# Optimization experiments

Measured on AMD Instinct MI355X. Metric: run time of the kernel, lower is better.

## Reference

```python
import jax, jax.numpy as jnp
import numpy as np

P = 1.0  # Yager t-norm exponent (tnorm_p)


def _patches(x, k):
    # x: [B, C, H, W] -> [B, C*k*k, Ho, Wo], feature ordering (c, kh, kw) like torch unfold
    B, C, H, W = x.shape
    Ho, Wo = H - k + 1, W - k + 1
    cols = [x[:, :, i:i + Ho, j:j + Wo] for i in range(k) for j in range(k)]
    p = jnp.stack(cols, axis=2)  # [B, C, k*k, Ho, Wo]
    return p.reshape(B, C * k * k, Ho, Wo)


def _max_yager2d(x, w, p):
    # Fuzzy conv: Yager t-norm T(a,b)=max(0, 1-((1-a)^p+(1-b)^p)^(1/p)) between each
    # patch element and kernel weight, aggregated with max over the receptive field.
    O, C, k, _ = w.shape
    pat = _patches(x, k)                       # [B, L, Ho, Wo], L = C*k*k
    wf = w.reshape(O, -1)                      # [O, L]
    a = 1.0 - pat[:, None]                     # [B, 1, L, Ho, Wo]
    b = 1.0 - wf[None, :, :, None, None]       # [1, O, L, 1, 1]
    t = jnp.maximum(0.0, 1.0 - (a ** p + b ** p) ** (1.0 / p))
    return jnp.max(t, axis=2)                  # [B, O, Ho, Wo]


def _maxpool2(x):
    return jax.lax.reduce_window(x, -jnp.inf, jax.lax.max,
                                 (1, 1, 2, 2), (1, 1, 2, 2), 'VALID')


def setup_inputs() -> dict:
    key = jax.random.key(0)
    k1, k2, k3, k4, k5, k6, k7 = jax.random.split(key, 7)
    B = 128
    inputs = jax.random.uniform(k1, (B, 3, 32, 32), dtype=jnp.float32)
    # fuzzy kernels are membership values in [0,1]
    w1 = jax.random.uniform(k2, (6, 3, 5, 5), dtype=jnp.float32)
    w2 = jax.random.uniform(k3, (16, 6, 5, 5), dtype=jnp.float32)
    w3 = jax.random.uniform(k4, (120, 16, 5, 5), dtype=jnp.float32)
    wd = jax.random.normal(k5, (120, 84), dtype=jnp.float32) * 0.1  # DenseDefuzzy weights
    wf = jax.random.normal(k6, (84, 10), dtype=jnp.float32) * 0.1   # fc5 weight
    bf = jax.random.normal(k7, (10,), dtype=jnp.float32) * 0.01     # fc5 bias
    return {"inputs": inputs, "w1": w1, "w2": w2, "w3": w3,
            "wd": wd, "wf": wf, "bf": bf}


def reference(inputs, w1, w2, w3, wd, wf, bf):
    x = _maxpool2(_max_yager2d(inputs, w1, P))   # [B,6,14,14]
    x = _maxpool2(_max_yager2d(x, w2, P))        # [B,16,5,5]
    x = _max_yager2d(x, w3, P)                   # [B,120,1,1]
    x = x.reshape(x.shape[0], -1)                # [B,120]
    x = jnp.tanh(x @ wd)                         # DenseDefuzzy (unnormalized) + tanh
    return jax.nn.log_softmax(x @ wf + bf, axis=-1)
```

## Files before the change

kernel.cpp:

```cpp
#include <hip/hip_runtime.h>
#include <math.h>


#define NT 1024
#define ROWS 34
#define PLANE (32 * ROWS)

__device__ __forceinline__ void bar_lds() {
    asm volatile("s_waitcnt lgkmcnt(0)" ::: "memory");
    __builtin_amdgcn_s_barrier();
    asm volatile("" ::: "memory");
}

__device__ __forceinline__ void dilate_row(const float* __restrict__ raw,
                                           int r, float* __restrict__ dst) {
    const int rA = (r > 0) ? r - 1 : 0;
    const int rB = (r < 5) ? r : 4;
    float t0 = fmaxf(raw[rA * 5 + 0], raw[rB * 5 + 0]);
    float t1 = fmaxf(raw[rA * 5 + 1], raw[rB * 5 + 1]);
    float t2 = fmaxf(raw[rA * 5 + 2], raw[rB * 5 + 2]);
    float t3 = fmaxf(raw[rA * 5 + 3], raw[rB * 5 + 3]);
    float t4 = fmaxf(raw[rA * 5 + 4], raw[rB * 5 + 4]);
    float2* d = (float2*)dst;
    d[0] = make_float2(t0, fmaxf(t0, t1));
    d[1] = make_float2(fmaxf(t1, t2), fmaxf(t2, t3));
    d[2] = make_float2(fmaxf(t3, t4), t4);
}

__global__ __launch_bounds__(NT) void fused_lenet(
    const float* __restrict__ x,
    const float* __restrict__ w1,
    const float* __restrict__ w2,
    const float* __restrict__ w3,
    const float* __restrict__ wd,
    const float* __restrict__ wf,
    const float* __restrict__ bfv,
    float* __restrict__ out)
{
    const int img = blockIdx.x;
    const int tid = threadIdx.x;

    __shared__ float s_in[3 * PLANE];
    __shared__ float s_w1d[648];
    __shared__ float s_w2d[3456];
    __shared__ float s_wf[850];
    __shared__ unsigned s_a1u[1176];
    __shared__ unsigned s_a2u[400];
    __shared__ float s_a3[120];
    __shared__ float s_a4[84];

    float4 w3p[13];

    {
        const float2* src = (const float2*)(x + img * 3072);
        for (int i = tid; i < 1536; i += NT) {
            const int c = i >> 9, rem = i & 511, r = rem >> 4, col2 = rem & 15;
            ((float2*)s_in)[c * (PLANE / 2) + r * (ROWS / 2) + col2] = src[i];
        }
        if (tid < 420) ((float2*)s_wf)[tid] = ((const float2*)wf)[tid];
        if (tid >= 428 && tid < 438) s_wf[840 + tid - 428] = bfv[tid - 428];
        for (int i = tid; i < 1176; i += NT) s_a1u[i] = 0u;
        if (tid < 400) s_a2u[tid] = 0u;
        if (tid >= 320 && tid < 428) {
            const int e = tid - 320;
            const int occ = e / 6, r = e - occ * 6;
            dilate_row(w1 + occ * 25, r, s_w1d + occ * 36 + r * 6);
        }
        if (tid >= 448) {
            const int e = tid - 448;
            const int occ = e / 6, r = e - occ * 6;
            dilate_row(w2 + occ * 25, r, s_w2d + occ * 36 + r * 6);
        }
    }
    bar_lds();

    if (tid < 336) {
        const int c = tid / 112;
        const int r = tid - c * 112;
        const int ocg = r / 56;
        const int r2 = r - ocg * 56;
        const int py = r2 >> 2;
        const int s = (r2 >> 1) & 1;
        const int h = r2 & 1;
        float acc[3][7];
        #pragma unroll
        for (int o = 0; o < 3; ++o)
            #pragma unroll
            for (int j = 0; j < 7; ++j) acc[o][j] = -1e30f;
        const float* xbase = s_in + c * PLANE + (2 * py + 3 * h) * ROWS + 14 * s;
        #pragma unroll
        for (int u = 0; u < 3; ++u) {
            float xv[18];
            #pragma unroll
            for (int i2 = 0; i2 < 9; ++i2)
                ((float2*)xv)[i2] = ((const float2*)(xbase + u * ROWS))[i2];
            #pragma unroll
            for (int o = 0; o < 3; ++o) {
                const float* wbase =
                    s_w1d + ((ocg * 3 + o) * 3 + c) * 36 + h * 18 + u * 6;
                float wv[6];
                #pragma unroll
                for (int i2 = 0; i2 < 3; ++i2)
                    ((float2*)wv)[i2] = ((const float2*)wbase)[i2];
                #pragma unroll
                for (int j = 0; j < 7; ++j) {
                    const float t0 = xv[2 * j + 0] + wv[0];
                    const float t1 = xv[2 * j + 1] + wv[1];
                    const float t2 = xv[2 * j + 2] + wv[2];
                    const float t3 = xv[2 * j + 3] + wv[3];
                    const float t4 = xv[2 * j + 4] + wv[4];
                    const float t5 = xv[2 * j + 5] + wv[5];
                    const float m1 = fmaxf(fmaxf(t0, t1), t2);
                    const float m2 = fmaxf(fmaxf(t3, t4), t5);
                    acc[o][j] = fmaxf(acc[o][j], fmaxf(m1, m2));
                }
            }
        }
        #pragma unroll
        for (int o = 0; o < 3; ++o) {
            const int obase = (ocg * 3 + o) * 196 + py * 14 + 7 * s;
            #pragma unroll
            for (int j = 0; j < 7; ++j) {
                const float rl = fmaxf(acc[o][j] - 1.0f, 0.0f);
                atomicMax(&s_a1u[obase + j], __float_as_uint(rl));
            }
        }
    }
    if (tid < 960) {
        const int o = tid >> 3, q = tid & 7;
        const float4* wv = (const float4*)(w3 + o * 400);
        #pragma unroll
        for (int i = 0; i < 13; ++i) {
            int l = q + 8 * i; if (l > 99) l = 99;
            w3p[i] = wv[l];
        }
    }
    bar_lds();

    if (tid < 240) {
        const int ocq = tid / 60;
        const int r = tid - ocq * 60;
        const int py = r / 12;
        const int r2 = r - py * 12;
        const int c = r2 >> 1;
        const int h = r2 & 1;
        float acc[4][5];
        #pragma unroll
        for (int o = 0; o < 4; ++o)
            #pragma unroll
            for (int j = 0; j < 5; ++j) acc[o][j] = -1e30f;
        const float* a1f = (const float*)s_a1u;
        const float* xbase = a1f + c * 196 + (2 * py + 3 * h) * 14;
        #pragma unroll
        for (int u = 0; u < 3; ++u) {
            float xv[14];
            #pragma unroll
            for (int i2 = 0; i2 < 7; ++i2)
                ((float2*)xv)[i2] = ((const float2*)(xbase + u * 14))[i2];
            #pragma unroll
            for (int o = 0; o < 4; ++o) {
                const float* wbase =
                    s_w2d + ((ocq * 4 + o) * 6 + c) * 36 + h * 18 + u * 6;
                float wv[6];
                #pragma unroll
                for (int i2 = 0; i2 < 3; ++i2)
                    ((float2*)wv)[i2] = ((const float2*)wbase)[i2];
                #pragma unroll
                for (int j = 0; j < 5; ++j) {
                    const float t0 = xv[2 * j + 0] + wv[0];
                    const float t1 = xv[2 * j + 1] + wv[1];
                    const float t2 = xv[2 * j + 2] + wv[2];
                    const float t3 = xv[2 * j + 3] + wv[3];
                    const float t4 = xv[2 * j + 4] + wv[4];
                    const float t5 = xv[2 * j + 5] + wv[5];
                    const float m1 = fmaxf(fmaxf(t0, t1), t2);
                    const float m2 = fmaxf(fmaxf(t3, t4), t5);
                    acc[o][j] = fmaxf(acc[o][j], fmaxf(m1, m2));
                }
            }
        }
        #pragma unroll
        for (int o = 0; o < 4; ++o) {
            const int obase = (ocq * 4 + o) * 25 + py * 5;
            #pragma unroll
            for (int j = 0; j < 5; ++j) {
                const float rl = fmaxf(acc[o][j] - 1.0f, 0.0f);
                atomicMax(&s_a2u[obase + j], __float_as_uint(rl));
            }
        }
    }
    float wdp[15];
    if (tid < 672) {
        const int o = tid >> 3, q = tid & 7;
        #pragma unroll
        for (int i = 0; i < 15; ++i)
            wdp[i] = wd[(q * 15 + i) * 84 + o];
    }
    bar_lds();

    if (tid < 960) {
        const int o = tid >> 3, q = tid & 7;
        const float4* av = (const float4*)(const float*)s_a2u;
        float m = -1e30f;
        #pragma unroll
        for (int i = 0; i < 13; ++i) {
            int l = q + 8 * i; if (l > 99) l = 99;
            const float4 a = av[l];
            const float4 w = w3p[i];
            m = fmaxf(m, fmaxf(fmaxf(a.x + w.x, a.y + w.y),
                               fmaxf(a.z + w.z, a.w + w.w)));
        }
        m = fmaxf(m, __shfl_xor(m, 1));
        m = fmaxf(m, __shfl_xor(m, 2));
        m = fmaxf(m, __shfl_xor(m, 4));
        if (q == 0) s_a3[o] = fmaxf(m - 1.0f, 0.0f);
    }
    bar_lds();

    if (tid < 672) {
        const int o = tid >> 3, q = tid & 7;
        float acc = 0.0f;
        #pragma unroll
        for (int i = 0; i < 15; ++i)
            acc = fmaf(s_a3[q * 15 + i], wdp[i], acc);
        acc += __shfl_xor(acc, 1);
        acc += __shfl_xor(acc, 2);
        acc += __shfl_xor(acc, 4);
        if (q == 0)
            s_a4[o] = 1.0f - 2.0f / (__expf(2.0f * acc) + 1.0f);
    }
    bar_lds();

    if (tid < 64) {
        float acc = 0.0f;
        if (tid < 40) {
            const int o = tid >> 2, q = tid & 3;
            #pragma unroll 7
            for (int i = 0; i < 21; ++i) {
                const int k = q * 21 + i;
                acc = fmaf(s_a4[k], s_wf[k * 10 + o], acc);
            }
            acc += __shfl_xor(acc, 1);
            acc += __shfl_xor(acc, 2);
            acc += s_wf[840 + o];
        }
        const float lg = __shfl(acc, (tid < 10) ? tid * 4 : 0);
        if (tid < 16) {
            float v = (tid < 10) ? lg : -1e30f;
            #pragma unroll
            for (int d = 1; d < 16; d <<= 1)
                v = fmaxf(v, __shfl_xor(v, d));
            float e = (tid < 10) ? __expf(lg - v) : 0.0f;
            float ssum = e;
            #pragma unroll
            for (int d = 1; d < 16; d <<= 1)
                ssum += __shfl_xor(ssum, d);
            if (tid < 10)
                out[img * 10 + tid] = lg - v - __logf(ssum);
        }
    }
}

extern "C" void kernel_launch(void* const* d_in, const int* in_sizes, int n_in,
                              void* d_out, int out_size, void* d_ws, size_t ws_size,
                              hipStream_t stream) {
    const float* x   = (const float*)d_in[0];
    const float* w1  = (const float*)d_in[1];
    const float* w2  = (const float*)d_in[2];
    const float* w3  = (const float*)d_in[3];
    const float* wd  = (const float*)d_in[4];
    const float* wf  = (const float*)d_in[5];
    const float* bfv = (const float*)d_in[6];
    float* out = (float*)d_out;

    const int B = in_sizes[0] / (3 * 32 * 32);
    fused_lenet<<<dim3(B), dim3(NT), 0, stream>>>(
        x, w1, w2, w3, wd, wf, bfv, out);
}
```

Measured before the change: 74.32 us.

## Replace LDS atomicMax reductions with DPP cross-lane max and reshape thread mapping

Conv1 and conv2 stages are remapped so the partial results that used to be merged with LDS atomicMax (over channels and kernel halves) now sit in adjacent lanes. They are combined with DPP quad-permute and row-shift max, and one lane writes the result directly. This drops the zero-initialisation of the accumulation buffers and the atomic traffic. It also swaps the shuffle-based reductions in the later layers for DPP, and pads the input plane stride. The cost is more active threads, some of them duplicated padding lanes, plus reliance on the row_shl semantics for the reduction pattern.

```diff
diff --git a/kernel.cpp b/kernel.cpp
--- a/kernel.cpp
+++ b/kernel.cpp
@@ -4,7 +4,23 @@
 
 #define NT 1024
 #define ROWS 34
-#define PLANE (32 * ROWS)
+#define PLANEF 1096
+
+#define QX1  0xB1
+#define QX2  0x4E
+#define SHL4 0x104
+#define SHL8 0x108
+
+template<int CTRL>
+__device__ __forceinline__ float dppmax(float v) {
+    int p = __builtin_amdgcn_update_dpp(0, __float_as_int(v), CTRL, 0xF, 0xF, true);
+    return fmaxf(v, __int_as_float(p));
+}
+template<int CTRL>
+__device__ __forceinline__ float dppadd(float v) {
+    int p = __builtin_amdgcn_update_dpp(0, __float_as_int(v), CTRL, 0xF, 0xF, true);
+    return v + __int_as_float(p);
+}
 
 __device__ __forceinline__ void bar_lds() {
     asm volatile("s_waitcnt lgkmcnt(0)" ::: "memory");
@@ -40,12 +56,12 @@
     const int img = blockIdx.x;
     const int tid = threadIdx.x;
 
-    __shared__ float s_in[3 * PLANE];
+    __shared__ __align__(16) float s_in[3 * PLANEF];
     __shared__ float s_w1d[648];
     __shared__ float s_w2d[3456];
-    __shared__ float s_wf[850];
-    __shared__ unsigned s_a1u[1176];
-    __shared__ unsigned s_a2u[400];
+    __shared__ __align__(16) float s_wf[852];
+    __shared__ __align__(16) float s_a1f[1176];
+    __shared__ __align__(16) float s_a2f[400];
     __shared__ float s_a3[120];
     __shared__ float s_a4[84];
 
@@ -55,12 +71,10 @@
         const float2* src = (const float2*)(x + img * 3072);
         for (int i = tid; i < 1536; i += NT) {
             const int c = i >> 9, rem = i & 511, r = rem >> 4, col2 = rem & 15;
-            ((float2*)s_in)[c * (PLANE / 2) + r * (ROWS / 2) + col2] = src[i];
+            ((float2*)s_in)[c * (PLANEF / 2) + r * (ROWS / 2) + col2] = src[i];
         }
         if (tid < 420) ((float2*)s_wf)[tid] = ((const float2*)wf)[tid];
         if (tid >= 428 && tid < 438) s_wf[840 + tid - 428] = bfv[tid - 428];
-        for (int i = tid; i < 1176; i += NT) s_a1u[i] = 0u;
-        if (tid < 400) s_a2u[tid] = 0u;
         if (tid >= 320 && tid < 428) {
             const int e = tid - 320;
             const int occ = e / 6, r = e - occ * 6;
@@ -74,20 +88,22 @@
     }
     bar_lds();
 
-    if (tid < 336) {
-        const int c = tid / 112;
-        const int r = tid - c * 112;
-        const int ocg = r / 56;
-        const int r2 = r - ocg * 56;
-        const int py = r2 >> 2;
-        const int s = (r2 >> 1) & 1;
-        const int h = r2 & 1;
+    if (tid < 448) {
+        const int l = tid & 7;
+        const int h = l & 1;
+        const int cc = l >> 1;
+        const int c = (cc < 3) ? cc : 2;
+        const int g = tid >> 3;
+        const int ocg = g / 28;
+        const int rem = g - ocg * 28;
+        const int py = rem >> 1;
+        const int s = rem & 1;
         float acc[3][7];
         #pragma unroll
         for (int o = 0; o < 3; ++o)
             #pragma unroll
             for (int j = 0; j < 7; ++j) acc[o][j] = -1e30f;
-        const float* xbase = s_in + c * PLANE + (2 * py + 3 * h) * ROWS + 14 * s;
+        const float* xbase = s_in + c * PLANEF + (2 * py + 3 * h) * ROWS + 14 * s;
         #pragma unroll
         for (int u = 0; u < 3; ++u) {
             float xv[18];
@@ -121,8 +137,10 @@
             const int obase = (ocg * 3 + o) * 196 + py * 14 + 7 * s;
             #pragma unroll
             for (int j = 0; j < 7; ++j) {
-                const float rl = fmaxf(acc[o][j] - 1.0f, 0.0f);
-                atomicMax(&s_a1u[obase + j], __float_as_uint(rl));
+                float v = dppmax<QX1>(acc[o][j]);
+                v = dppmax<QX2>(v);
+                v = dppmax<SHL4>(v);
+                if (l == 0) s_a1f[obase + j] = fmaxf(v - 1.0f, 0.0f);
             }
         }
     }
@@ -131,26 +149,26 @@
         const float4* wv = (const float4*)(w3 + o * 400);
         #pragma unroll
         for (int i = 0; i < 13; ++i) {
-            int l = q + 8 * i; if (l > 99) l = 99;
-            w3p[i] = wv[l];
-        }
-    }
-    bar_lds();
-
-    if (tid < 240) {
-        const int ocq = tid / 60;
-        const int r = tid - ocq * 60;
-        const int py = r / 12;
-        const int r2 = r - py * 12;
-        const int c = r2 >> 1;
-        const int h = r2 & 1;
+            int l2 = q + 8 * i; if (l2 > 99) l2 = 99;
+            w3p[i] = wv[l2];
+        }
+    }
+    bar_lds();
+
+    if (tid < 320) {
+        const int l = tid & 15;
+        const int h = l & 1;
+        const int cc = l >> 1;
+        const int c = (cc < 6) ? cc : 5;
+        const int g = tid >> 4;
+        const int ocq = g / 5;
+        const int py = g - ocq * 5;
         float acc[4][5];
         #pragma unroll
         for (int o = 0; o < 4; ++o)
             #pragma unroll
             for (int j = 0; j < 5; ++j) acc[o][j] = -1e30f;
-        const float* a1f = (const float*)s_a1u;
-        const float* xbase = a1f + c * 196 + (2 * py + 3 * h) * 14;
+        const float* xbase = s_a1f + c * 196 + (2 * py + 3 * h) * 14;
         #pragma unroll
         for (int u = 0; u < 3; ++u) {
             float xv[14];
@@ -184,8 +202,11 @@
             const int obase = (ocq * 4 + o) * 25 + py * 5;
             #pragma unroll
             for (int j = 0; j < 5; ++j) {
-                const float rl = fmaxf(acc[o][j] - 1.0f, 0.0f);
-                atomicMax(&s_a2u[obase + j], __float_as_uint(rl));
+                float v = dppmax<QX1>(acc[o][j]);
+                v = dppmax<QX2>(v);
+                v = dppmax<SHL4>(v);
+                v = dppmax<SHL8>(v);
+                if (l == 0) s_a2f[obase + j] = fmaxf(v - 1.0f, 0.0f);
             }
         }
     }
@@ -200,19 +221,19 @@
 
     if (tid < 960) {
         const int o = tid >> 3, q = tid & 7;
-        const float4* av = (const float4*)(const float*)s_a2u;
+        const float4* av = (const float4*)s_a2f;
         float m = -1e30f;
         #pragma unroll
         for (int i = 0; i < 13; ++i) {
-            int l = q + 8 * i; if (l > 99) l = 99;
-            const float4 a = av[l];
+            int l2 = q + 8 * i; if (l2 > 99) l2 = 99;
+            const float4 a = av[l2];
             const float4 w = w3p[i];
             m = fmaxf(m, fmaxf(fmaxf(a.x + w.x, a.y + w.y),
                                fmaxf(a.z + w.z, a.w + w.w)));
         }
-        m = fmaxf(m, __shfl_xor(m, 1));
-        m = fmaxf(m, __shfl_xor(m, 2));
-        m = fmaxf(m, __shfl_xor(m, 4));
+        m = dppmax<QX1>(m);
+        m = dppmax<QX2>(m);
+        m = dppmax<SHL4>(m);
         if (q == 0) s_a3[o] = fmaxf(m - 1.0f, 0.0f);
     }
     bar_lds();
@@ -223,9 +244,9 @@
         #pragma unroll
         for (int i = 0; i < 15; ++i)
             acc = fmaf(s_a3[q * 15 + i], wdp[i], acc);
-        acc += __shfl_xor(acc, 1);
-        acc += __shfl_xor(acc, 2);
-        acc += __shfl_xor(acc, 4);
+        acc = dppadd<QX1>(acc);
+        acc = dppadd<QX2>(acc);
+        acc = dppadd<SHL4>(acc);
         if (q == 0)
             s_a4[o] = 1.0f - 2.0f / (__expf(2.0f * acc) + 1.0f);
     }
```

New measurement: 94.14 us. +26.7%, slower.
